# Kernel tuning notes

Hardware: AMD Instinct MI355X
Metric: run time of the kernel (lower is better)

The kernel has to match this reference:

```python
import jax, jax.numpy as jnp
import numpy as np

S, K, O = 8192, 1024, 4096  # seq_len, in_features, out_features


def setup_inputs() -> dict:
    key = jax.random.key(0)
    k1, k2, k3, k4, k5 = jax.random.split(key, 5)
    x = jax.random.randint(k1, (S, K), -128, 128, dtype=jnp.int8)
    weight_q = jax.random.randint(k2, (O, K), -128, 128, dtype=jnp.int8)
    scale_x = jax.random.uniform(k3, (), jnp.float32, 0.01, 0.1)
    scale_w = jax.random.uniform(k4, (), jnp.float32, 0.01, 0.1)
    scale_y = jax.random.uniform(k5, (S,), jnp.float32, 0.5, 2.0)  # per-row output scale
    return {"x": x, "weight_q": weight_q, "scale_x": scale_x,
            "scale_w": scale_w, "scale_y": scale_y}


def reference(x, weight_q, scale_x, scale_w, scale_y):
    # int8 GEMM with int32 accumulation: [S,K] @ [O,K]^T -> [S,O]
    acc = jnp.einsum('sk,ok->so', x.astype(jnp.int32), weight_q.astype(jnp.int32))
    # fused per-row requantization: scale_y[:seq_len] gives per-row scale
    requant_scale = (scale_x * scale_w / scale_y).astype(jnp.float32)  # [S]
    scaled = acc.astype(jnp.float32) * requant_scale[:, None]
    out_q = jnp.clip(jnp.round(scaled), -128.0, 127.0).astype(jnp.int8)
    return out_q, scale_y
```

## Files before the change

kernel.cpp:

```cpp
#include <hip/hip_runtime.h>


#define S_DIM 8192
#define K_DIM 1024
#define O_DIM 4096
#define BM 128
#define BN 128
#define BK 64

using i32x4 = __attribute__((ext_vector_type(4))) int;

__device__ __forceinline__ void load_lds16(const void* g, void* l) {
  __builtin_amdgcn_global_load_lds(
      (const __attribute__((address_space(1))) void*)g,
      (__attribute__((address_space(3))) void*)l, 16, 0, 0);
}

__global__ void pack_kernel(const int* __restrict__ xi, const int* __restrict__ wi,
                            const float* __restrict__ sy,
                            unsigned int* __restrict__ xq, unsigned int* __restrict__ wq,
                            float* __restrict__ out_sy) {
  const int idx = blockIdx.x * blockDim.x + threadIdx.x;
  const int nx = S_DIM * K_DIM / 4;
  const int nw = O_DIM * K_DIM / 4;
  if (idx < nx) {
    int4 v = ((const int4*)xi)[idx];
    unsigned int p = (v.x & 0xff) | ((v.y & 0xff) << 8) |
                     ((v.z & 0xff) << 16) | ((unsigned)(v.w & 0xff) << 24);
    xq[idx] = p;
  } else if (idx < nx + nw) {
    const int j = idx - nx;
    int4 v = ((const int4*)wi)[j];
    unsigned int p = (v.x & 0xff) | ((v.y & 0xff) << 8) |
                     ((v.z & 0xff) << 16) | ((unsigned)(v.w & 0xff) << 24);
    wq[j] = p;
  }
  if (idx < S_DIM) out_sy[idx] = sy[idx];
}

__global__ __launch_bounds__(256) void gemm_i8_kernel(
    const signed char* __restrict__ A,
    const signed char* __restrict__ B,
    const float* __restrict__ sx, const float* __restrict__ sw,
    const float* __restrict__ sy, float* __restrict__ out) {
  __shared__ __align__(16) signed char As[BM * BK];
  __shared__ __align__(16) signed char Bs[BN * BK];

  const int tid = threadIdx.x;
  const int wave = tid >> 6;
  const int lane = tid & 63;
  const int wm = wave >> 1;
  const int wn = wave & 1;
  const int rowBase = blockIdx.y * BM;
  const int colBase = blockIdx.x * BN;

  const int sRow = wave * 16 + (lane >> 2);
  const int sCol = (lane & 3) * 16;
  const signed char* gA = A + (size_t)(rowBase + sRow) * K_DIM + sCol;
  const signed char* gB = B + (size_t)(colBase + sRow) * K_DIM + sCol;
  signed char* lA = As + wave * 1024;
  signed char* lB = Bs + wave * 1024;

  i32x4 acc[4][4] = {};

  const int fr = lane & 15;
  const int fq = (lane >> 4) * 16;

  for (int k0 = 0; k0 < K_DIM; k0 += BK) {
    load_lds16(gA + k0, lA);
    load_lds16(gA + (size_t)64 * K_DIM + k0, lA + 4096);
    load_lds16(gB + k0, lB);
    load_lds16(gB + (size_t)64 * K_DIM + k0, lB + 4096);
    __syncthreads();

    i32x4 af[4], bf[4];
#pragma unroll
    for (int mi = 0; mi < 4; ++mi)
      af[mi] = *(const i32x4*)(As + (wm * 64 + mi * 16 + fr) * BK + fq);
#pragma unroll
    for (int ni = 0; ni < 4; ++ni)
      bf[ni] = *(const i32x4*)(Bs + (wn * 64 + ni * 16 + fr) * BK + fq);

#pragma unroll
    for (int mi = 0; mi < 4; ++mi)
#pragma unroll
      for (int ni = 0; ni < 4; ++ni)
        acc[mi][ni] =
            __builtin_amdgcn_mfma_i32_16x16x64_i8(af[mi], bf[ni], acc[mi][ni], 0, 0, 0);
    __syncthreads();
  }

  const float sxw = sx[0] * sw[0];
  const int quad = lane >> 4;
#pragma unroll
  for (int mi = 0; mi < 4; ++mi) {
#pragma unroll
    for (int r = 0; r < 4; ++r) {
      const int s = rowBase + wm * 64 + mi * 16 + quad * 4 + r;
      const float rs = sxw / sy[s];
      float* orow = out + (size_t)s * O_DIM + colBase + wn * 64 + fr;
#pragma unroll
      for (int ni = 0; ni < 4; ++ni) {
        float f = rintf((float)acc[mi][ni][r] * rs);
        f = fminf(127.0f, fmaxf(-128.0f, f));
        orow[ni * 16] = f;
      }
    }
  }
}

extern "C" void kernel_launch(void* const* d_in, const int* in_sizes, int n_in,
                              void* d_out, int out_size, void* d_ws, size_t ws_size,
                              hipStream_t stream) {
  const int* x = (const int*)d_in[0];
  const int* w = (const int*)d_in[1];
  const float* sx = (const float*)d_in[2];
  const float* sw = (const float*)d_in[3];
  const float* sy = (const float*)d_in[4];
  float* out = (float*)d_out;

  unsigned int* xq = (unsigned int*)d_ws;
  unsigned int* wq = xq + (size_t)S_DIM * K_DIM / 4;

  const int total = S_DIM * K_DIM / 4 + O_DIM * K_DIM / 4;
  pack_kernel<<<(total + 255) / 256, 256, 0, stream>>>(
      x, w, sy, xq, wq, out + (size_t)S_DIM * O_DIM);

  dim3 grid(O_DIM / BN, S_DIM / BM);
  gemm_i8_kernel<<<grid, 256, 0, stream>>>(
      (const signed char*)xq, (const signed char*)wq, sx, sw, sy, out);
}
```

Baseline: 204.3 us.

## Load MFMA fragments directly from global memory, dropping LDS staging and barriers

Removes the shared-memory tiles and global_load_lds staging, so each wave reads its A and B MFMA fragments straight from global memory (through the caches) every K step. This drops both __syncthreads per iteration, and the launch bounds now request 4 blocks per SM with the K loop unrolled by 2 so loads can overlap. The cost is that data reuse across waves now depends on L1/L2 rather than LDS, which doubles global load requests, and each lane reads strided 16-byte rows.

```diff
diff --git a/kernel.cpp b/kernel.cpp
--- a/kernel.cpp
+++ b/kernel.cpp
@@ -9,12 +9,6 @@
 #define BK 64
 
 using i32x4 = __attribute__((ext_vector_type(4))) int;
-
-__device__ __forceinline__ void load_lds16(const void* g, void* l) {
-  __builtin_amdgcn_global_load_lds(
-      (const __attribute__((address_space(1))) void*)g,
-      (__attribute__((address_space(3))) void*)l, 16, 0, 0);
-}
 
 __global__ void pack_kernel(const int* __restrict__ xi, const int* __restrict__ wi,
                             const float* __restrict__ sy,
@@ -38,14 +32,11 @@
   if (idx < S_DIM) out_sy[idx] = sy[idx];
 }
 
-__global__ __launch_bounds__(256) void gemm_i8_kernel(
+__global__ __launch_bounds__(256, 4) void gemm_i8_kernel(
     const signed char* __restrict__ A,
     const signed char* __restrict__ B,
     const float* __restrict__ sx, const float* __restrict__ sw,
     const float* __restrict__ sy, float* __restrict__ out) {
-  __shared__ __align__(16) signed char As[BM * BK];
-  __shared__ __align__(16) signed char Bs[BN * BK];
-
   const int tid = threadIdx.x;
   const int wave = tid >> 6;
   const int lane = tid & 63;
@@ -54,32 +45,23 @@
   const int rowBase = blockIdx.y * BM;
   const int colBase = blockIdx.x * BN;
 
-  const int sRow = wave * 16 + (lane >> 2);
-  const int sCol = (lane & 3) * 16;
-  const signed char* gA = A + (size_t)(rowBase + sRow) * K_DIM + sCol;
-  const signed char* gB = B + (size_t)(colBase + sRow) * K_DIM + sCol;
-  signed char* lA = As + wave * 1024;
-  signed char* lB = Bs + wave * 1024;
+  const int fr = lane & 15;
+  const int kq = (lane >> 4) * 16;
+
+  const signed char* pA = A + (size_t)(rowBase + wm * 64 + fr) * K_DIM + kq;
+  const signed char* pB = B + (size_t)(colBase + wn * 64 + fr) * K_DIM + kq;
 
   i32x4 acc[4][4] = {};
 
-  const int fr = lane & 15;
-  const int fq = (lane >> 4) * 16;
-
+#pragma unroll 2
   for (int k0 = 0; k0 < K_DIM; k0 += BK) {
-    load_lds16(gA + k0, lA);
-    load_lds16(gA + (size_t)64 * K_DIM + k0, lA + 4096);
-    load_lds16(gB + k0, lB);
-    load_lds16(gB + (size_t)64 * K_DIM + k0, lB + 4096);
-    __syncthreads();
-
     i32x4 af[4], bf[4];
 #pragma unroll
     for (int mi = 0; mi < 4; ++mi)
-      af[mi] = *(const i32x4*)(As + (wm * 64 + mi * 16 + fr) * BK + fq);
+      af[mi] = *(const i32x4*)(pA + (size_t)mi * 16 * K_DIM + k0);
 #pragma unroll
     for (int ni = 0; ni < 4; ++ni)
-      bf[ni] = *(const i32x4*)(Bs + (wn * 64 + ni * 16 + fr) * BK + fq);
+      bf[ni] = *(const i32x4*)(pB + (size_t)ni * 16 * K_DIM + k0);
 
 #pragma unroll
     for (int mi = 0; mi < 4; ++mi)
@@ -87,7 +69,6 @@
       for (int ni = 0; ni < 4; ++ni)
         acc[mi][ni] =
             __builtin_amdgcn_mfma_i32_16x16x64_i8(af[mi], bf[ni], acc[mi][ni], 0, 0, 0);
-    __syncthreads();
   }
 
   const float sxw = sx[0] * sw[0];
```

New measurement: 281.4 us. +37.8%, slower.

## Double-buffer LDS tiles to overlap global loads with MFMA compute

Applied to the files above, without the earlier changes.

Splits the A and B LDS tiles into two buffers. The next K-tile's global-to-LDS loads are issued before computing on the current buffer, and the second barrier per iteration is removed. This is meant to hide global load latency behind MFMA work. It doubles LDS use to 32KB per block, and it adds a launch_bounds occupancy hint of 4 blocks. Correctness depends on the single barrier ordering reuse of each buffer, and on the asynchronous LDS loads finishing before that barrier.

```diff
diff --git a/kernel.cpp b/kernel.cpp
--- a/kernel.cpp
+++ b/kernel.cpp
@@ -7,6 +7,7 @@
 #define BM 128
 #define BN 128
 #define BK 64
+#define NITER (K_DIM / BK)
 
 using i32x4 = __attribute__((ext_vector_type(4))) int;
 
@@ -38,13 +39,13 @@
   if (idx < S_DIM) out_sy[idx] = sy[idx];
 }
 
-__global__ __launch_bounds__(256) void gemm_i8_kernel(
+__global__ __launch_bounds__(256, 4) void gemm_i8_kernel(
     const signed char* __restrict__ A,
     const signed char* __restrict__ B,
     const float* __restrict__ sx, const float* __restrict__ sw,
     const float* __restrict__ sy, float* __restrict__ out) {
-  __shared__ __align__(16) signed char As[BM * BK];
-  __shared__ __align__(16) signed char Bs[BN * BK];
+  __shared__ __align__(16) signed char As[2][BM * BK];
+  __shared__ __align__(16) signed char Bs[2][BN * BK];
 
   const int tid = threadIdx.x;
   const int wave = tid >> 6;
@@ -58,28 +59,44 @@
   const int sCol = (lane & 3) * 16;
   const signed char* gA = A + (size_t)(rowBase + sRow) * K_DIM + sCol;
   const signed char* gB = B + (size_t)(colBase + sRow) * K_DIM + sCol;
-  signed char* lA = As + wave * 1024;
-  signed char* lB = Bs + wave * 1024;
 
   i32x4 acc[4][4] = {};
 
   const int fr = lane & 15;
   const int fq = (lane >> 4) * 16;
 
-  for (int k0 = 0; k0 < K_DIM; k0 += BK) {
-    load_lds16(gA + k0, lA);
-    load_lds16(gA + (size_t)64 * K_DIM + k0, lA + 4096);
-    load_lds16(gB + k0, lB);
-    load_lds16(gB + (size_t)64 * K_DIM + k0, lB + 4096);
+  {
+    signed char* lA = As[0] + wave * 1024;
+    signed char* lB = Bs[0] + wave * 1024;
+    load_lds16(gA, lA);
+    load_lds16(gA + (size_t)64 * K_DIM, lA + 4096);
+    load_lds16(gB, lB);
+    load_lds16(gB + (size_t)64 * K_DIM, lB + 4096);
+  }
+
+  for (int it = 0; it < NITER; ++it) {
     __syncthreads();
 
+    if (it + 1 < NITER) {
+      const int nb = (it + 1) & 1;
+      const int k0 = (it + 1) * BK;
+      signed char* lA = As[nb] + wave * 1024;
+      signed char* lB = Bs[nb] + wave * 1024;
+      load_lds16(gA + k0, lA);
+      load_lds16(gA + (size_t)64 * K_DIM + k0, lA + 4096);
+      load_lds16(gB + k0, lB);
+      load_lds16(gB + (size_t)64 * K_DIM + k0, lB + 4096);
+    }
+
+    const signed char* curA = As[it & 1];
+    const signed char* curB = Bs[it & 1];
     i32x4 af[4], bf[4];
 #pragma unroll
     for (int mi = 0; mi < 4; ++mi)
-      af[mi] = *(const i32x4*)(As + (wm * 64 + mi * 16 + fr) * BK + fq);
+      af[mi] = *(const i32x4*)(curA + (wm * 64 + mi * 16 + fr) * BK + fq);
 #pragma unroll
     for (int ni = 0; ni < 4; ++ni)
-      bf[ni] = *(const i32x4*)(Bs + (wn * 64 + ni * 16 + fr) * BK + fq);
+      bf[ni] = *(const i32x4*)(curB + (wn * 64 + ni * 16 + fr) * BK + fq);
 
 #pragma unroll
     for (int mi = 0; mi < 4; ++mi)
@@ -87,7 +104,6 @@
       for (int ni = 0; ni < 4; ++ni)
         acc[mi][ni] =
             __builtin_amdgcn_mfma_i32_16x16x64_i8(af[mi], bf[ni], acc[mi][ni], 0, 0, 0);
-    __syncthreads();
   }
 
   const float sxw = sx[0] * sw[0];
```

Result: no change. 203.8 us (-0.2%).
